# Kernel optimization log

Measured on AMD Instinct MI355X. Metric: run time of the kernel, lower is better.

## Reference

```python
import jax, jax.numpy as jnp
import numpy as np

B, S, H, L, NH, V = 8, 512, 768, 12, 12, 21128
DH = H // NH
FF = 4 * H
PAD_ID, SEP_ID = 0, 102
EPS = 1e-12


def _ln(x, g, b):
    mu = jnp.mean(x, axis=-1, keepdims=True)
    var = jnp.mean(jnp.square(x - mu), axis=-1, keepdims=True)
    return (x - mu) * jax.lax.rsqrt(var + EPS) * g + b


def setup_inputs() -> dict:
    key = jax.random.key(0)
    ks = jax.random.split(key, 24)
    # token ids with a per-sample [SEP] boundary and trailing padding
    ids = jax.random.randint(ks[0], (B, S), 1, V)
    qpos = jax.random.randint(ks[1], (B,), 16, 64)
    seqlen = jax.random.randint(ks[2], (B,), 384, S + 1)
    pos = jnp.arange(S)
    ids = jnp.where(pos[None, :] == qpos[:, None], SEP_ID, ids)
    ids = jnp.where(pos[None, :] < seqlen[:, None], ids, PAD_ID)

    w = lambda k, shape: (jax.random.normal(k, shape, dtype=jnp.float32) * 0.02)
    return {
        "input_ids": ids,
        "word_emb": w(ks[3], (V, H)),
        "pos_emb": w(ks[4], (S, H)),
        "type_emb": w(ks[5], (2, H)),
        "emb_ln_g": jnp.ones((H,), jnp.float32),
        "emb_ln_b": jnp.zeros((H,), jnp.float32),
        "attn_w": w(ks[6], (L, 4, H, H)),     # q,k,v,o projections
        "attn_b": w(ks[7], (L, 4, H)),
        "ln1_g": jnp.ones((L, H), jnp.float32),
        "ln1_b": jnp.zeros((L, H), jnp.float32),
        "ffn_w1": w(ks[8], (L, H, FF)),
        "ffn_b1": w(ks[9], (L, FF)),
        "ffn_w2": w(ks[10], (L, FF, H)),
        "ffn_b2": w(ks[11], (L, H)),
        "ln2_g": jnp.ones((L, H), jnp.float32),
        "ln2_b": jnp.zeros((L, H), jnp.float32),
        "cls_w": w(ks[12], (H, V)),
        "cls_b": jnp.zeros((V,), jnp.float32),
    }


def _qa_causal_bias(input_ids):
    # Faithful to make_qa_causal_mask: pad mask * (bidirectional over question,
    # causal over answer), boundary = first [SEP] position + 1 per sample.
    pad = input_ids != PAD_ID                                  # [B,S]
    qlen = jnp.argmax(input_ids == SEP_ID, axis=1) + 1          # [B]
    i = jnp.arange(S)[:, None]
    j = jnp.arange(S)[None, :]
    in_answer = (i[None] >= qlen[:, None, None]) & (j[None] >= qlen[:, None, None])
    causal_ok = jnp.where(in_answer, j <= i, True)              # [B,S,S]
    mask = pad[:, :, None] & pad[:, None, :] & causal_ok
    return jnp.where(mask, 0.0, -1e9).astype(jnp.float32)       # additive bias


def reference(input_ids, word_emb, pos_emb, type_emb, emb_ln_g, emb_ln_b,
              attn_w, attn_b, ln1_g, ln1_b, ffn_w1, ffn_b1, ffn_w2, ffn_b2,
              ln2_g, ln2_b, cls_w, cls_b):
    bias = _qa_causal_bias(input_ids)[:, None]                  # [B,1,S,S]
    h = word_emb[input_ids] + pos_emb[None, :S] + type_emb[0]
    h = _ln(h, emb_ln_g, emb_ln_b)
    scale = 1.0 / jnp.sqrt(jnp.float32(DH))
    for l in range(L):
        wq, wk, wv, wo = attn_w[l]
        bq, bk, bv, bo = attn_b[l]
        q = (h @ wq + bq).reshape(B, S, NH, DH)
        k = (h @ wk + bk).reshape(B, S, NH, DH)
        v = (h @ wv + bv).reshape(B, S, NH, DH)
        scores = jnp.einsum('bqhd,bkhd->bhqk', q, k) * scale + bias
        probs = jax.nn.softmax(scores, axis=-1)
        ctx = jnp.einsum('bhqk,bkhd->bqhd', probs, v).reshape(B, S, H)
        h = _ln(h + ctx @ wo + bo, ln1_g[l], ln1_b[l])
        ff = jax.nn.gelu(h @ ffn_w1[l] + ffn_b1[l], approximate=False) @ ffn_w2[l] + ffn_b2[l]
        h = _ln(h + ff, ln2_g[l], ln2_b[l])
    return h @ cls_w + cls_b                                    # [B,S,V] logits
```

## Files before the change

kernel.cpp:

```cpp
#include <hip/hip_runtime.h>
#include <hip/hip_bf16.h>
#include <stdint.h>

#define BB   8
#define SS   512
#define HH   768
#define LL   12
#define NHH  12
#define DHH  64
#define FFF  3072
#define VV   21128
#define PAD_ID 0
#define SEP_ID 102
#define BS   (BB*SS)
#define BSH  ((size_t)BS*HH)
#define BSFF ((size_t)BS*FFF)
#define QKVN (3*HH)

using bf16 = __hip_bfloat16;
typedef __attribute__((ext_vector_type(8))) short short8;
typedef __attribute__((ext_vector_type(4))) short short4v;
typedef __attribute__((ext_vector_type(4))) float f32x4;

__device__ __forceinline__ f32x4 Z4() { f32x4 z = {0.f, 0.f, 0.f, 0.f}; return z; }

__device__ __forceinline__ void gload16(void* lds, const void* g) {
    __builtin_amdgcn_global_load_lds(
        (const __attribute__((address_space(1))) uint32_t*)g,
        (__attribute__((address_space(3))) uint32_t*)(uint32_t)(uintptr_t)lds,
        16, 0, 0);
}

template <int N>
__device__ __forceinline__ void waitvm() {
    if constexpr (N == 0) asm volatile("s_waitcnt vmcnt(0)" ::: "memory");
    else if constexpr (N == 2) asm volatile("s_waitcnt vmcnt(2)" ::: "memory");
    else if constexpr (N == 3) asm volatile("s_waitcnt vmcnt(3)" ::: "memory");
    else if constexpr (N == 4) asm volatile("s_waitcnt vmcnt(4)" ::: "memory");
    else if constexpr (N == 6) asm volatile("s_waitcnt vmcnt(6)" ::: "memory");
    else asm volatile("s_waitcnt vmcnt(8)" ::: "memory");
    __builtin_amdgcn_sched_barrier(0);
}

__device__ __forceinline__ void barrier_raw() {
    __builtin_amdgcn_s_barrier();
    __builtin_amdgcn_sched_barrier(0);
}

__device__ __forceinline__ void wait_vm0_lgkm0_barrier() {
    asm volatile("s_waitcnt vmcnt(0) lgkmcnt(0)" ::: "memory");
    __builtin_amdgcn_sched_barrier(0);
    __builtin_amdgcn_s_barrier();
    __builtin_amdgcn_sched_barrier(0);
}

__global__ void __launch_bounds__(256) qlen_kernel(const int* __restrict__ ids,
                                                   int* __restrict__ qlen) {
    int b = blockIdx.x, tid = threadIdx.x;
    __shared__ int red[256];
    int best = 1 << 30;
    for (int j = tid; j < SS; j += 256)
        if (ids[b * SS + j] == SEP_ID) best = min(best, j);
    red[tid] = best; __syncthreads();
    for (int off = 128; off > 0; off >>= 1) {
        if (tid < off) red[tid] = min(red[tid], red[tid + off]);
        __syncthreads();
    }
    if (tid == 0) qlen[b] = (red[0] == (1 << 30) ? 0 : red[0]) + 1;
}

__device__ __forceinline__ float block_reduce_sum(float v, float* red, int tid) {
    red[tid] = v; __syncthreads();
    for (int off = 128; off > 0; off >>= 1) {
        if (tid < off) red[tid] += red[tid + off];
        __syncthreads();
    }
    float r = red[0]; __syncthreads();
    return r;
}

__global__ void __launch_bounds__(256) embed_ln_kernel(
    const int* __restrict__ ids, const float* __restrict__ we,
    const float* __restrict__ pe, const float* __restrict__ te,
    const float* __restrict__ g, const float* __restrict__ bt,
    float* __restrict__ h, bf16* __restrict__ hb) {
    int token = blockIdx.x, tid = threadIdx.x;
    int s = token % SS;
    int id = ids[token];
    __shared__ float red[256];
    float x[3];
#pragma unroll
    for (int i = 0; i < 3; ++i) {
        int idx = tid + i * 256;
        x[i] = we[(size_t)id * HH + idx] + pe[(size_t)s * HH + idx] + te[idx];
    }
    float sum = block_reduce_sum(x[0] + x[1] + x[2], red, tid);
    float mu = sum * (1.0f / HH);
    float vs = 0.f;
#pragma unroll
    for (int i = 0; i < 3; ++i) { float d = x[i] - mu; vs += d * d; }
    vs = block_reduce_sum(vs, red, tid);
    float rstd = rsqrtf(vs * (1.0f / HH) + 1e-12f);
    size_t base = (size_t)token * HH;
#pragma unroll
    for (int i = 0; i < 3; ++i) {
        int idx = tid + i * 256;
        float v = (x[i] - mu) * rstd * g[idx] + bt[idx];
        h[base + idx] = v;
        hb[base + idx] = __float2bfloat16(v);
    }
}

__global__ void __launch_bounds__(256) add_ln_kernel(
    float* __restrict__ h, const float* __restrict__ proj,
    const float* __restrict__ proj2,
    const float* __restrict__ g, const float* __restrict__ bt,
    bf16* __restrict__ hb) {
    int token = blockIdx.x, tid = threadIdx.x;
    __shared__ float red[256];
    size_t base = (size_t)token * HH;
    float x[3];
#pragma unroll
    for (int i = 0; i < 3; ++i) {
        int idx = tid + i * 256;
        x[i] = h[base + idx] + proj[base + idx] + proj2[base + idx];
    }
    float sum = block_reduce_sum(x[0] + x[1] + x[2], red, tid);
    float mu = sum * (1.0f / HH);
    float vs = 0.f;
#pragma unroll
    for (int i = 0; i < 3; ++i) { float d = x[i] - mu; vs += d * d; }
    vs = block_reduce_sum(vs, red, tid);
    float rstd = rsqrtf(vs * (1.0f / HH) + 1e-12f);
#pragma unroll
    for (int i = 0; i < 3; ++i) {
        int idx = tid + i * 256;
        float v = (x[i] - mu) * rstd * g[idx] + bt[idx];
        h[base + idx] = v;
        hb[base + idx] = __float2bfloat16(v);
    }
}

__global__ void __launch_bounds__(256) transp_conv(
    const float* __restrict__ in, bf16* __restrict__ out,
    int K, int N, size_t inStride, size_t outStride) {
    const float* src = in + (size_t)blockIdx.z * inStride;
    bf16* dst = out + (size_t)blockIdx.z * outStride;
    __shared__ float t[64][65];
    int n0 = blockIdx.x * 64, k0 = blockIdx.y * 64;
    int tid = threadIdx.x;
    int r = tid >> 4, c4 = (tid & 15) * 4;
#pragma unroll
    for (int i = 0; i < 4; ++i) {
        int kk = k0 + r + i * 16;
        int n = n0 + c4;
        float4 v;
        if (n + 3 < N) {
            v = *(const float4*)(src + (size_t)kk * N + n);
        } else {
            v.x = (n + 0 < N) ? src[(size_t)kk * N + n + 0] : 0.f;
            v.y = (n + 1 < N) ? src[(size_t)kk * N + n + 1] : 0.f;
            v.z = (n + 2 < N) ? src[(size_t)kk * N + n + 2] : 0.f;
            v.w = (n + 3 < N) ? src[(size_t)kk * N + n + 3] : 0.f;
        }
        t[c4 + 0][r + i * 16] = v.x;
        t[c4 + 1][r + i * 16] = v.y;
        t[c4 + 2][r + i * 16] = v.z;
        t[c4 + 3][r + i * 16] = v.w;
    }
    __syncthreads();
#pragma unroll
    for (int i = 0; i < 4; ++i) {
        int nn = n0 + r + i * 16;
        if (nn < N) {
            short4v o;
            o[0] = (short)__bfloat16_as_ushort(__float2bfloat16(t[r + i * 16][c4 + 0]));
            o[1] = (short)__bfloat16_as_ushort(__float2bfloat16(t[r + i * 16][c4 + 1]));
            o[2] = (short)__bfloat16_as_ushort(__float2bfloat16(t[r + i * 16][c4 + 2]));
            o[3] = (short)__bfloat16_as_ushort(__float2bfloat16(t[r + i * 16][c4 + 3]));
            *(short4v*)(dst + (size_t)nn * K + k0 + c4) = o;
        }
    }
}

__global__ void __launch_bounds__(256) vtrans_kernel(const bf16* __restrict__ v,
                                                     bf16* __restrict__ vT,
                                                     int ldv) {
    __shared__ bf16 t[64][68];
    int s0 = blockIdx.x * 64, h = blockIdx.y, b = blockIdx.z;
    int tid = threadIdx.x;
    int r = tid >> 4, c4 = (tid & 15) * 4;
#pragma unroll
    for (int i = 0; i < 4; ++i) {
        int sr = r + i * 16;
        short4v x = *(const short4v*)(v + ((size_t)(b * SS + s0 + sr)) * ldv +
                                      h * 64 + c4);
        t[c4 + 0][sr] = __ushort_as_bfloat16((unsigned short)x[0]);
        t[c4 + 1][sr] = __ushort_as_bfloat16((unsigned short)x[1]);
        t[c4 + 2][sr] = __ushort_as_bfloat16((unsigned short)x[2]);
        t[c4 + 3][sr] = __ushort_as_bfloat16((unsigned short)x[3]);
    }
    __syncthreads();
#pragma unroll
    for (int i = 0; i < 4; ++i) {
        int dr = r + i * 16;
        short4v o;
        o[0] = (short)__bfloat16_as_ushort(t[dr][c4 + 0]);
        o[1] = (short)__bfloat16_as_ushort(t[dr][c4 + 1]);
        o[2] = (short)__bfloat16_as_ushort(t[dr][c4 + 2]);
        o[3] = (short)__bfloat16_as_ushort(t[dr][c4 + 3]);
        *(short4v*)(vT + (((size_t)(b * NHH + h)) * 64 + dr) * SS + s0 + c4) = o;
    }
}

#define GBK 32

template <int THREADS, int TBM, int TBN, int OUT_BF16, int ACT, int KK,
          int LDA, int LDB, int LDC, int NN, int NSTAGES>
__global__ void __launch_bounds__(THREADS) gemm_bf16_kernel(
    const bf16* __restrict__ A, const bf16* __restrict__ BT,
    const float* __restrict__ bias, void* __restrict__ Cout, size_t zStride) {
    constexpr int WN = (THREADS == 512) ? 4 : 2;
    constexpr int WM = 2;
    constexpr int MFRAG = TBM / WM / 16;
    constexpr int NFRAG = TBN / WN / 16;
    constexpr int ABYTES = TBM * GBK * 2;
    constexpr int BBYTES = TBN * GBK * 2;
    constexpr int A_ISS = ABYTES / (THREADS * 16);
    constexpr int B_ISS = BBYTES / (THREADS * 16);
    constexpr int LPS = A_ISS + B_ISS;
    __shared__ __align__(16) char smem[NSTAGES * (ABYTES + BBYTES)];
    char* Asm = smem;
    char* Bsm = smem + NSTAGES * ABYTES;
    int tid = threadIdx.x;
    int lane = tid & 63, wid = tid >> 6;

    int zz = blockIdx.z;
    const char* Ab = (const char*)(A + (size_t)zz * KK);
    const char* Bb = (const char*)(BT + (size_t)zz * KK);

    int gN = gridDim.x, gM = gridDim.y;
    int nwg = gN * gM;
    int bid = blockIdx.y * gN + blockIdx.x;
    int swz = ((nwg & 7) == 0) ? ((bid & 7) * (nwg >> 3) + (bid >> 3)) : bid;
    int width = 8 * gN;
    int grp = swz / width, rem = swz % width;
    int gh = min(8, gM - grp * 8);
    int by = grp * 8 + rem % gh;
    int bx = rem / gh;

    int m0 = by * TBM, n0 = bx * TBN;
    int wr = (wid / WN) * (TBM / WM);
    int wc = (wid % WN) * (TBN / WN);

    f32x4 acc[MFRAG][NFRAG];
#pragma unroll
    for (int i = 0; i < MFRAG; ++i)
#pragma unroll
        for (int j = 0; j < NFRAG; ++j) acc[i][j] = Z4();

    auto stage = [&](int k0, int sel) {
#pragma unroll
        for (int i = 0; i < A_ISS; ++i) {
            int lin = tid * 16 + i * (THREADS * 16);
            int row = lin >> 6, slot = (lin >> 4) & 3;
            gload16(Asm + sel * ABYTES + lin,
                    Ab + ((size_t)(m0 + row) * LDA + k0) * 2 +
                        ((slot ^ ((row >> 1) & 3)) << 4));
        }
#pragma unroll
        for (int i = 0; i < B_ISS; ++i) {
            int lin = tid * 16 + i * (THREADS * 16);
            int row = lin >> 6, slot = (lin >> 4) & 3;
            int nr = n0 + row;
            if constexpr (NN % TBN != 0) { if (nr >= NN) nr = NN - 1; }
            gload16(Bsm + sel * BBYTES + lin,
                    Bb + ((size_t)nr * LDB + k0) * 2 +
                        ((slot ^ ((row >> 1) & 3)) << 4));
        }
    };

    constexpr int T = KK / GBK;
#pragma unroll
    for (int s = 0; s < NSTAGES - 1; ++s) stage(s * GBK, s);
    waitvm<(NSTAGES - 2) * LPS>();
    barrier_raw();

    for (int t = 0; t < T; ++t) {
        if (t + NSTAGES - 1 < T)
            stage((t + NSTAGES - 1) * GBK, (t + NSTAGES - 1) % NSTAGES);

        const char* Ar = Asm + (t % NSTAGES) * ABYTES;
        const char* Br = Bsm + (t % NSTAGES) * BBYTES;
        short8 af[MFRAG], bfr[NFRAG];
#pragma unroll
        for (int i = 0; i < MFRAG; ++i) {
            int ar = wr + i * 16 + (lane & 15);
            int slot = (lane >> 4) ^ ((ar >> 1) & 3);
            af[i] = *(const short8*)(Ar + ar * 64 + slot * 16);
        }
#pragma unroll
        for (int j = 0; j < NFRAG; ++j) {
            int br = wc + j * 16 + (lane & 15);
            int slot = (lane >> 4) ^ ((br >> 1) & 3);
            bfr[j] = *(const short8*)(Br + br * 64 + slot * 16);
        }
#pragma unroll
        for (int i = 0; i < MFRAG; ++i)
#pragma unroll
            for (int j = 0; j < NFRAG; ++j)
                acc[i][j] = __builtin_amdgcn_mfma_f32_16x16x32_bf16(
                    af[i], bfr[j], acc[i][j], 0, 0, 0);

        if (t + 1 < T) {
            if (t + 2 < T) waitvm<LPS>();
            else           waitvm<0>();
            barrier_raw();
        }
    }

    bool nfull = (NN % TBN == 0) || (n0 + TBN <= NN);
#pragma unroll
    for (int i = 0; i < MFRAG; ++i) {
#pragma unroll
        for (int r = 0; r < 4; ++r) {
            int m = m0 + wr + i * 16 + (lane >> 4) * 4 + r;
#pragma unroll
            for (int j = 0; j < NFRAG; ++j) {
                int n = n0 + wc + j * 16 + (lane & 15);
                if (nfull || n < NN) {
                    float v = acc[i][j][r] + ((zz == 0) ? bias[n] : 0.f);
                    if (ACT) v = 0.5f * v * (1.0f + erff(v * 0.70710678118654752f));
                    if (OUT_BF16)
                        ((bf16*)Cout)[(size_t)m * LDC + n] = __float2bfloat16(v);
                    else
                        ((float*)Cout)[zz * zStride + (size_t)m * LDC + n] = v;
                }
            }
        }
    }
}

__global__ void __launch_bounds__(256) attn_mfma_kernel(
    const bf16* __restrict__ Q, const bf16* __restrict__ K,
    const bf16* __restrict__ VT, const int* __restrict__ ids,
    const int* __restrict__ qlen, bf16* __restrict__ att, int ld) {
    __shared__ __align__(16) bf16 Qs[64 * 64];
    __shared__ __align__(16) bf16 Ks[2][64 * 64];
    __shared__ __align__(16) bf16 Vs[2][64 * 64];
    __shared__ __align__(16) bf16 Ps[4 * 16 * 64];
    __shared__ float padj[2][64];

    int tid = threadIdx.x, lane = tid & 63, w = tid >> 6;
    int q0 = blockIdx.x * 64, h = blockIdx.y, b = blockIdx.z;
    int ql = qlen[b];

    const char* kbase0 = (const char*)K + ((size_t)(b * SS) * ld) * 2;
    const char* vbase0 = (const char*)VT + (((size_t)(b * NHH + h)) * 64) * SS * 2;

    auto stageKV = [&](int kv0, int sel) {
        int lin = tid * 16;
#pragma unroll
        for (int i = 0; i < 2; ++i, lin += 4096) {
            int row = lin >> 7, bir = lin & 127;
            int sbir = bir ^ ((row & 7) << 4);
            gload16((char*)Ks[sel] + lin,
                    kbase0 + (size_t)(kv0 + row) * (ld * 2) + h * 128 + sbir);
            gload16((char*)Vs[sel] + lin,
                    vbase0 + (size_t)row * (SS * 2) + (size_t)kv0 * 2 + sbir);
        }
        if (tid < 64)
            padj[sel][tid] = (ids[b * SS + kv0 + tid] != PAD_ID) ? 1.f : 0.f;
    };

    {
        const char* qbase =
            (const char*)Q + ((size_t)(b * SS + q0) * ld) * 2 + h * 128;
        int lin = tid * 16;
#pragma unroll
        for (int i = 0; i < 2; ++i, lin += 4096) {
            int row = lin >> 7, bir = lin & 127;
            int sbir = bir ^ ((row & 7) << 4);
            gload16((char*)Qs + lin, qbase + (size_t)row * (ld * 2) + sbir);
        }
    }
    stageKV(0, 0);
    int qrow_base = q0 + w * 16 + (lane >> 4) * 4;
    bool padq[4];
#pragma unroll
    for (int r = 0; r < 4; ++r)
        padq[r] = (ids[b * SS + qrow_base + r] != PAD_ID);

    wait_vm0_lgkm0_barrier();

    short8 aq[2];
#pragma unroll
    for (int ks = 0; ks < 2; ++ks) {
        int row = w * 16 + (lane & 15);
        int bir = ks * 64 + (lane >> 4) * 16;
        aq[ks] = *(const short8*)((const char*)Qs + row * 128 +
                                  (bir ^ ((row & 7) << 4)));
    }

    float m_run[4], l_run[4];
    f32x4 accO[4];
#pragma unroll
    for (int r = 0; r < 4; ++r) { m_run[r] = -1e30f; l_run[r] = 0.f; }
#pragma unroll
    for (int d = 0; d < 4; ++d) accO[d] = Z4();

    int cur = 0;
    for (int kv0 = 0; kv0 < SS; kv0 += 64) {
        if (kv0 + 64 < SS) stageKV(kv0 + 64, cur ^ 1);
        const char* kb = (const char*)Ks[cur];
        const char* vb = (const char*)Vs[cur];

        f32x4 accS[4];
        __builtin_amdgcn_s_setprio(1);
#pragma unroll
        for (int nf = 0; nf < 4; ++nf) {
            f32x4 z = Z4();
#pragma unroll
            for (int ks = 0; ks < 2; ++ks) {
                int row = nf * 16 + (lane & 15);
                int bir = ks * 64 + (lane >> 4) * 16;
                short8 bk = *(const short8*)(kb + row * 128 +
                                             (bir ^ ((row & 7) << 4)));
                z = __builtin_amdgcn_mfma_f32_16x16x32_bf16(aq[ks], bk, z, 0, 0, 0);
            }
            accS[nf] = z;
        }
        __builtin_amdgcn_s_setprio(0);

        float p[4][4];
#pragma unroll
        for (int r = 0; r < 4; ++r) {
            int qg = qrow_base + r;
            float mx = -1e30f;
#pragma unroll
            for (int nf = 0; nf < 4; ++nf) {
                int j = kv0 + nf * 16 + (lane & 15);
                bool ok = padq[r] && (padj[cur][nf * 16 + (lane & 15)] != 0.f) &&
                          ((qg < ql) || (j < ql) || (j <= qg));
                float s = accS[nf][r] * 0.125f + (ok ? 0.f : -1e9f);
                p[r][nf] = s;
                mx = fmaxf(mx, s);
            }
#pragma unroll
            for (int off = 1; off < 16; off <<= 1)
                mx = fmaxf(mx, __shfl_xor(mx, off));
            float mnew = fmaxf(m_run[r], mx);
            float fac = __expf(m_run[r] - mnew);
            m_run[r] = mnew;
            float rs = 0.f;
#pragma unroll
            for (int nf = 0; nf < 4; ++nf) {
                float e = __expf(p[r][nf] - mnew);
                p[r][nf] = e;
                rs += e;
            }
#pragma unroll
            for (int off = 1; off < 16; off <<= 1)
                rs += __shfl_xor(rs, off);
            l_run[r] = l_run[r] * fac + rs;
#pragma unroll
            for (int df = 0; df < 4; ++df) accO[df][r] *= fac;
        }

#pragma unroll
        for (int r = 0; r < 4; ++r) {
            int prow = (lane >> 4) * 4 + r;
#pragma unroll
            for (int nf = 0; nf < 4; ++nf) {
                int c = nf * 16 + (lane & 15);
                int byte = (c * 2) ^ ((prow & 7) << 4);
                *(bf16*)((char*)Ps + w * 2048 + prow * 128 + byte) =
                    __float2bfloat16(p[r][nf]);
            }
        }
        asm volatile("s_waitcnt lgkmcnt(0)" ::: "memory");
        __builtin_amdgcn_sched_barrier(0);

        __builtin_amdgcn_s_setprio(1);
#pragma unroll
        for (int ks = 0; ks < 2; ++ks) {
            int prow = lane & 15;
            int bir = ks * 64 + (lane >> 4) * 16;
            short8 ap = *(const short8*)((const char*)Ps + w * 2048 + prow * 128 +
                                         (bir ^ ((prow & 7) << 4)));
#pragma unroll
            for (int df = 0; df < 4; ++df) {
                int vrow = df * 16 + (lane & 15);
                short8 bv = *(const short8*)(vb + vrow * 128 +
                                             (bir ^ ((vrow & 7) << 4)));
                accO[df] = __builtin_amdgcn_mfma_f32_16x16x32_bf16(
                    ap, bv, accO[df], 0, 0, 0);
            }
        }
        __builtin_amdgcn_s_setprio(0);

        if (kv0 + 64 < SS) wait_vm0_lgkm0_barrier();
        cur ^= 1;
    }

#pragma unroll
    for (int r = 0; r < 4; ++r) {
        int qg = qrow_base + r;
        float inv = 1.0f / l_run[r];
#pragma unroll
        for (int df = 0; df < 4; ++df) {
            int d = df * 16 + (lane & 15);
            att[((size_t)(b * SS) + qg) * HH + h * 64 + d] =
                __float2bfloat16(accO[df][r] * inv);
        }
    }
}

extern "C" void kernel_launch(void* const* d_in, const int* in_sizes, int n_in,
                              void* d_out, int out_size, void* d_ws, size_t ws_size,
                              hipStream_t stream) {
    const int*   ids      = (const int*)d_in[0];
    const float* word_emb = (const float*)d_in[1];
    const float* pos_emb  = (const float*)d_in[2];
    const float* type_emb = (const float*)d_in[3];
    const float* emb_ln_g = (const float*)d_in[4];
    const float* emb_ln_b = (const float*)d_in[5];
    const float* attn_w   = (const float*)d_in[6];
    const float* attn_b   = (const float*)d_in[7];
    const float* ln1_g    = (const float*)d_in[8];
    const float* ln1_b    = (const float*)d_in[9];
    const float* ffn_w1   = (const float*)d_in[10];
    const float* ffn_b1   = (const float*)d_in[11];
    const float* ffn_w2   = (const float*)d_in[12];
    const float* ffn_b2   = (const float*)d_in[13];
    const float* ln2_g    = (const float*)d_in[14];
    const float* ln2_b    = (const float*)d_in[15];
    const float* cls_w    = (const float*)d_in[16];
    const float* cls_b    = (const float*)d_in[17];
    float* out = (float*)d_out;

    char* base = (char*)d_ws;
    size_t off = 0;
    auto take = [&](size_t bytes) {
        char* r = base + off;
        off += (bytes + 255) & ~(size_t)255;
        return r;
    };
    float* h    = (float*)take(BSH * 4);
    float* proj = (float*)take(2 * BSH * 4);
    bf16*  qkv  = (bf16*)take((size_t)BS * QKVN * 2);
    bf16*  vT   = (bf16*)take(BSH * 2);
    bf16*  attb = (bf16*)take(BSH * 2);
    bf16*  ffb  = (bf16*)take(BSFF * 2);
    bf16*  hb   = (bf16*)take(BSH * 2);
    int*   qlen = (int*)take(256);
    size_t commonEnd = off;

    const size_t szAttnW = (size_t)48 * HH * HH * 2;
    const size_t szW1    = (size_t)LL * HH * FFF * 2;
    const size_t szCls   = (size_t)VV * HH * 2;
    const size_t fullNeed = commonEnd + szAttnW + 2 * szW1 + szCls;
    bool fullMode = (ws_size >= fullNeed);

    bf16 *wAttnT = nullptr, *w1T = nullptr, *w2T = nullptr, *clsT = nullptr, *wrot = nullptr;
    if (fullMode) {
        wAttnT = (bf16*)take(szAttnW);
        w1T    = (bf16*)take(szW1);
        w2T    = (bf16*)take(szW1);
        clsT   = (bf16*)take(szCls);
    } else {
        wrot = (bf16*)take((size_t)HH * FFF * 2);
        clsT = (bf16*)proj;
    }

    auto convw = [&](const float* src, bf16* dst, int K, int N) {
        dim3 g((N + 63) / 64, K / 64, 1);
        transp_conv<<<g, 256, 0, stream>>>(src, dst, K, N, (size_t)0, (size_t)0);
    };

    qlen_kernel<<<BB, 256, 0, stream>>>(ids, qlen);

    if (fullMode) {
        transp_conv<<<dim3(12, 12, 48), 256, 0, stream>>>(
            attn_w, wAttnT, HH, HH, (size_t)HH * HH, (size_t)HH * HH);
        transp_conv<<<dim3(FFF / 64, HH / 64, LL), 256, 0, stream>>>(
            ffn_w1, w1T, HH, FFF, (size_t)HH * FFF, (size_t)HH * FFF);
        transp_conv<<<dim3(HH / 64, FFF / 64, LL), 256, 0, stream>>>(
            ffn_w2, w2T, FFF, HH, (size_t)HH * FFF, (size_t)HH * FFF);
        transp_conv<<<dim3((VV + 63) / 64, HH / 64, 1), 256, 0, stream>>>(
            cls_w, clsT, HH, VV, (size_t)0, (size_t)0);
    }

    embed_ln_kernel<<<BS, 256, 0, stream>>>(ids, word_emb, pos_emb, type_emb,
                                            emb_ln_g, emb_ln_b, h, hb);

    dim3 gQKV(QKVN / 128, BS / 128, 1);
    dim3 gWo(HH / 64, BS / 128, 2);
    dim3 gFF1(FFF / 128, BS / 128, 1);
    dim3 gFF2(HH / 64, BS / 128, 2);
    dim3 gCls((VV + 127) / 128, BS / 128, 1);
    dim3 gAttn(SS / 64, NHH, BB);
    dim3 gVT(SS / 64, NHH, BB);

    for (int l = 0; l < LL; ++l) {
        const float* wq32 = attn_w + (size_t)l * 4 * HH * HH;
        const float* wo32 = wq32 + (size_t)3 * HH * HH;
        const float* bqkv = attn_b + (size_t)l * 4 * HH;
        const float* bo   = bqkv + 3 * HH;

        bf16 *wqkvT, *woT, *w1Tl, *w2Tl;
        if (fullMode) {
            wqkvT = wAttnT + (size_t)(l * 4) * HH * HH;
            woT   = wAttnT + (size_t)(l * 4 + 3) * HH * HH;
            w1Tl  = w1T + (size_t)l * HH * FFF;
            w2Tl  = w2T + (size_t)l * HH * FFF;
        } else {
            wqkvT = woT = w1Tl = w2Tl = wrot;
        }

        if (!fullMode) {
            convw(wq32, wrot, HH, HH);
            convw(wq32 + (size_t)HH * HH, wrot + (size_t)HH * HH, HH, HH);
            convw(wq32 + (size_t)2 * HH * HH, wrot + (size_t)2 * HH * HH, HH, HH);
        }
        gemm_bf16_kernel<512, 128, 128, 1, 0, HH, HH, HH, QKVN, QKVN, 3>
            <<<gQKV, 512, 0, stream>>>(hb, wqkvT, bqkv, qkv, 0);

        vtrans_kernel<<<gVT, 256, 0, stream>>>(qkv + 2 * HH, vT, QKVN);
        attn_mfma_kernel<<<gAttn, 256, 0, stream>>>(
            qkv, qkv + HH, vT, ids, qlen, attb, QKVN);

        if (!fullMode) convw(wo32, wrot, HH, HH);
        gemm_bf16_kernel<256, 128, 64, 0, 0, HH / 2, HH, HH, HH, HH, 3>
            <<<gWo, 256, 0, stream>>>(attb, woT, bo, proj, BSH);
        add_ln_kernel<<<BS, 256, 0, stream>>>(h, proj, proj + BSH,
                                              ln1_g + (size_t)l * HH,
                                              ln1_b + (size_t)l * HH, hb);

        if (!fullMode) convw(ffn_w1 + (size_t)l * HH * FFF, wrot, HH, FFF);
        gemm_bf16_kernel<512, 128, 128, 1, 1, HH, HH, HH, FFF, FFF, 3>
            <<<gFF1, 512, 0, stream>>>(hb, w1Tl, ffn_b1 + (size_t)l * FFF, ffb, 0);
        if (!fullMode) convw(ffn_w2 + (size_t)l * HH * FFF, wrot, FFF, HH);
        gemm_bf16_kernel<256, 128, 64, 0, 0, FFF / 2, FFF, FFF, HH, HH, 3>
            <<<gFF2, 256, 0, stream>>>(ffb, w2Tl, ffn_b2 + (size_t)l * HH, proj,
                                       BSH);
        add_ln_kernel<<<BS, 256, 0, stream>>>(h, proj, proj + BSH,
                                              ln2_g + (size_t)l * HH,
                                              ln2_b + (size_t)l * HH, hb);
    }

    if (!fullMode) convw(cls_w, clsT, HH, VV);
    gemm_bf16_kernel<512, 128, 128, 0, 0, HH, HH, HH, VV, VV, 3>
        <<<gCls, 512, 0, stream>>>(hb, clsT, cls_b, out, 0);
}
```

Before: 2.638 ms.

## Add 256x256-tile bf16 GEMM kernel for QKV, FFN1 and classifier projections

Introduces a new GEMM kernel with 256x256 output tiles, BK=64, double-buffered XOR-swizzled LDS, grouped block swizzling for L2 locality, and staged loads interleaved with MFMA phases. It replaces the 128x128 kernel for the QKV, FFN1 and classifier GEMMs to raise arithmetic intensity and cut global/LDS traffic per FLOP. The trade-offs are 128KB of LDS per block and large accumulator register use, fewer blocks for the smaller GEMMs (QKV yields only 144 blocks), and some wasted tile work on the ragged vocab edge.

```diff
diff --git a/kernel.cpp b/kernel.cpp
--- a/kernel.cpp
+++ b/kernel.cpp
@@ -211,6 +211,129 @@
         o[3] = (short)__bfloat16_as_ushort(t[dr][c4 + 3]);
         *(short4v*)(vT + (((size_t)(b * NHH + h)) * 64 + dr) * SS + s0 + c4) = o;
     }
+}
+
+template <int OUT_BF16, int ACT, int KK, int LDA, int LDB, int LDC, int NN>
+__global__ void __launch_bounds__(512, 2) gemm256_kernel(
+    const bf16* __restrict__ A, const bf16* __restrict__ BT,
+    const float* __restrict__ bias, void* __restrict__ Cout) {
+    __shared__ __align__(16) char smem[2 * 65536];
+    int tid = threadIdx.x, lane = tid & 63, wid = tid >> 6;
+    int mg = wid >> 2, ng = wid & 3;
+
+    int gN = gridDim.x, gM = gridDim.y;
+    int nwg = gN * gM;
+    int bid = blockIdx.y * gN + blockIdx.x;
+    int swz = ((nwg & 7) == 0) ? ((bid & 7) * (nwg >> 3) + (bid >> 3)) : bid;
+    int width = 8 * gN;
+    int grp = swz / width, rem = swz % width;
+    int gh = min(8, gM - grp * 8);
+    int by = grp * 8 + rem % gh;
+    int bx = rem / gh;
+    int m0 = by * 256, n0 = bx * 256;
+
+    const char* Ab = (const char*)A;
+    const char* Bb = (const char*)BT;
+
+    f32x4 acc[4][2][4];
+#pragma unroll
+    for (int p = 0; p < 4; ++p)
+#pragma unroll
+        for (int i = 0; i < 2; ++i)
+#pragma unroll
+            for (int j = 0; j < 4; ++j) acc[p][i][j] = Z4();
+
+    auto stageChunk = [&](int k0, int sel, int ch) {
+        const bool isB = (ch & 1);
+        const int hr0 = (ch >> 1) * 128;
+        char* base = smem + sel * 65536 + (isB ? 32768 : 0) + hr0 * 128;
+#pragma unroll
+        for (int i = 0; i < 2; ++i) {
+            int lin = tid * 16 + i * 8192;
+            int srow = hr0 + (lin >> 7);
+            int so = ((((lin >> 4) & 7) ^ (srow & 7)) << 4);
+            if (!isB) {
+                gload16(base + lin,
+                        Ab + ((size_t)(m0 + srow) * LDA + k0) * 2 + so);
+            } else {
+                int nr = n0 + srow;
+                if constexpr (NN % 256 != 0) { if (nr >= NN) nr = NN - 1; }
+                gload16(base + lin,
+                        Bb + ((size_t)nr * LDB + k0) * 2 + so);
+            }
+        }
+    };
+
+    auto ldfrag = [&](const char* buf, int row, int ks) -> short8 {
+        int slot = ks * 4 + (lane >> 4);
+        return *(const short8*)(buf + row * 128 + ((slot ^ (row & 7)) << 4));
+    };
+
+    constexpr int T = KK / 64;
+#pragma unroll
+    for (int ch = 0; ch < 4; ++ch) stageChunk(0, 0, ch);
+
+    for (int t = 0; t < T; ++t) {
+        const char* Abuf = smem + (t & 1) * 65536;
+        const char* Bbuf = Abuf + 32768;
+        short8 bfr[4][2];
+#pragma unroll
+        for (int p = 0; p < 4; ++p) {
+            if (p == 0) waitvm<0>();
+            barrier_raw();
+            short8 af[2][2];
+#pragma unroll
+            for (int i = 0; i < 2; ++i)
+#pragma unroll
+                for (int ks = 0; ks < 2; ++ks)
+                    af[i][ks] = ldfrag(
+                        Abuf, mg * 128 + p * 32 + i * 16 + (lane & 15), ks);
+            if (p == 0) {
+#pragma unroll
+                for (int j = 0; j < 4; ++j)
+#pragma unroll
+                    for (int ks = 0; ks < 2; ++ks)
+                        bfr[j][ks] = ldfrag(
+                            Bbuf, ng * 64 + j * 16 + (lane & 15), ks);
+            }
+            if (t + 1 < T) stageChunk((t + 1) * 64, (t + 1) & 1, p);
+            asm volatile("s_waitcnt lgkmcnt(0)" ::: "memory");
+            __builtin_amdgcn_sched_barrier(0);
+            __builtin_amdgcn_s_setprio(1);
+#pragma unroll
+            for (int ks = 0; ks < 2; ++ks)
+#pragma unroll
+                for (int i = 0; i < 2; ++i)
+#pragma unroll
+                    for (int j = 0; j < 4; ++j)
+                        acc[p][i][j] = __builtin_amdgcn_mfma_f32_16x16x32_bf16(
+                            af[i][ks], bfr[j][ks], acc[p][i][j], 0, 0, 0);
+            __builtin_amdgcn_s_setprio(0);
+        }
+    }
+
+#pragma unroll
+    for (int p = 0; p < 4; ++p)
+#pragma unroll
+        for (int i = 0; i < 2; ++i)
+#pragma unroll
+            for (int r = 0; r < 4; ++r) {
+                int m = m0 + mg * 128 + p * 32 + i * 16 + (lane >> 4) * 4 + r;
+#pragma unroll
+                for (int j = 0; j < 4; ++j) {
+                    int n = n0 + ng * 64 + j * 16 + (lane & 15);
+                    if ((NN % 256 == 0) || n < NN) {
+                        float v = acc[p][i][j][r] + bias[n];
+                        if (ACT)
+                            v = 0.5f * v * (1.0f + erff(v * 0.70710678118654752f));
+                        if (OUT_BF16)
+                            ((bf16*)Cout)[(size_t)m * LDC + n] =
+                                __float2bfloat16(v);
+                        else
+                            ((float*)Cout)[(size_t)m * LDC + n] = v;
+                    }
+                }
+            }
 }
 
 #define GBK 32
@@ -594,11 +717,11 @@
     embed_ln_kernel<<<BS, 256, 0, stream>>>(ids, word_emb, pos_emb, type_emb,
                                             emb_ln_g, emb_ln_b, h, hb);
 
-    dim3 gQKV(QKVN / 128, BS / 128, 1);
+    dim3 gQKV(QKVN / 256, BS / 256, 1);
     dim3 gWo(HH / 64, BS / 128, 2);
-    dim3 gFF1(FFF / 128, BS / 128, 1);
+    dim3 gFF1(FFF / 256, BS / 256, 1);
     dim3 gFF2(HH / 64, BS / 128, 2);
-    dim3 gCls((VV + 127) / 128, BS / 128, 1);
+    dim3 gCls((VV + 255) / 256, BS / 256, 1);
     dim3 gAttn(SS / 64, NHH, BB);
     dim3 gVT(SS / 64, NHH, BB);
 
@@ -623,8 +746,8 @@
             convw(wq32 + (size_t)HH * HH, wrot + (size_t)HH * HH, HH, HH);
             convw(wq32 + (size_t)2 * HH * HH, wrot + (size_t)2 * HH * HH, HH, HH);
         }
-        gemm_bf16_kernel<512, 128, 128, 1, 0, HH, HH, HH, QKVN, QKVN, 3>
-            <<<gQKV, 512, 0, stream>>>(hb, wqkvT, bqkv, qkv, 0);
+        gemm256_kernel<1, 0, HH, HH, HH, QKVN, QKVN>
+            <<<gQKV, 512, 0, stream>>>(hb, wqkvT, bqkv, qkv);
 
         vtrans_kernel<<<gVT, 256, 0, stream>>>(qkv + 2 * HH, vT, QKVN);
         attn_mfma_kernel<<<gAttn, 256, 0, stream>>>(
@@ -638,8 +761,8 @@
                                               ln1_b + (size_t)l * HH, hb);
 
         if (!fullMode) convw(ffn_w1 + (size_t)l * HH * FFF, wrot, HH, FFF);
-        gemm_bf16_kernel<512, 128, 128, 1, 1, HH, HH, HH, FFF, FFF, 3>
-            <<<gFF1, 512, 0, stream>>>(hb, w1Tl, ffn_b1 + (size_t)l * FFF, ffb, 0);
+        gemm256_kernel<1, 1, HH, HH, HH, FFF, FFF>
+            <<<gFF1, 512, 0, stream>>>(hb, w1Tl, ffn_b1 + (size_t)l * FFF, ffb);
         if (!fullMode) convw(ffn_w2 + (size_t)l * HH * FFF, wrot, FFF, HH);
         gemm_bf16_kernel<256, 128, 64, 0, 0, FFF / 2, FFF, FFF, HH, HH, 3>
             <<<gFF2, 256, 0, stream>>>(ffb, w2Tl, ffn_b2 + (size_t)l * HH, proj,
@@ -650,6 +773,6 @@
     }
 
     if (!fullMode) convw(cls_w, clsT, HH, VV);
-    gemm_bf16_kernel<512, 128, 128, 0, 0, HH, HH, HH, VV, VV, 3>
-        <<<gCls, 512, 0, stream>>>(hb, clsT, cls_b, out, 0);
-}
+    gemm256_kernel<0, 0, HH, HH, HH, VV, VV>
+        <<<gCls, 512, 0, stream>>>(hb, clsT, cls_b, out);
+}
```

After: 2.692 ms. +2.1%, slower.

## Add 256x256 four-stage GEMM for classifier and wave-per-token add+LayerNorm

Applied to the files above, without the earlier changes.

Adds a dedicated GEMM kernel with 256x256 output tiles, a 4-buffer cp-async style pipeline, XOR-swizzled LDS and grouped block swizzling, and uses it for the large vocabulary classifier projection. Larger tiles raise arithmetic intensity and cut redundant A/B loads for the big N=21128 output. Separately, the add+LayerNorm kernel now handles one token per wavefront with float4 loads and shuffle reductions instead of block-level shared-memory reductions. The bigger tile uses more LDS and registers, which limits occupancy to one block per CU, and the ragged N edge is handled with clamped loads and masked stores.

```diff
diff --git a/kernel.cpp b/kernel.cpp
--- a/kernel.cpp
+++ b/kernel.cpp
@@ -116,28 +116,46 @@
     const float* __restrict__ proj2,
     const float* __restrict__ g, const float* __restrict__ bt,
     bf16* __restrict__ hb) {
-    int token = blockIdx.x, tid = threadIdx.x;
-    __shared__ float red[256];
-    size_t base = (size_t)token * HH;
-    float x[3];
+    int tid = threadIdx.x, lane = tid & 63, w = tid >> 6;
+    size_t token = (size_t)blockIdx.x * 4 + w;
+    size_t base = token * HH;
+    f32x4 x[3];
+    float s = 0.f;
 #pragma unroll
     for (int i = 0; i < 3; ++i) {
-        int idx = tid + i * 256;
-        x[i] = h[base + idx] + proj[base + idx] + proj2[base + idx];
-    }
-    float sum = block_reduce_sum(x[0] + x[1] + x[2], red, tid);
-    float mu = sum * (1.0f / HH);
+        int j = (lane + i * 64) * 4;
+        f32x4 a = *(const f32x4*)(h + base + j);
+        f32x4 b = *(const f32x4*)(proj + base + j);
+        f32x4 c = *(const f32x4*)(proj2 + base + j);
+        f32x4 v = a + b + c;
+        x[i] = v;
+        s += v[0] + v[1] + v[2] + v[3];
+    }
+#pragma unroll
+    for (int off = 1; off < 64; off <<= 1) s += __shfl_xor(s, off);
+    float mu = s * (1.0f / HH);
     float vs = 0.f;
 #pragma unroll
-    for (int i = 0; i < 3; ++i) { float d = x[i] - mu; vs += d * d; }
-    vs = block_reduce_sum(vs, red, tid);
+    for (int i = 0; i < 3; ++i)
+#pragma unroll
+        for (int e = 0; e < 4; ++e) { float d = x[i][e] - mu; vs += d * d; }
+#pragma unroll
+    for (int off = 1; off < 64; off <<= 1) vs += __shfl_xor(vs, off);
     float rstd = rsqrtf(vs * (1.0f / HH) + 1e-12f);
 #pragma unroll
     for (int i = 0; i < 3; ++i) {
-        int idx = tid + i * 256;
-        float v = (x[i] - mu) * rstd * g[idx] + bt[idx];
-        h[base + idx] = v;
-        hb[base + idx] = __float2bfloat16(v);
+        int j = (lane + i * 64) * 4;
+        f32x4 gg = *(const f32x4*)(g + j);
+        f32x4 bb = *(const f32x4*)(bt + j);
+        f32x4 y;
+        short4v yb;
+#pragma unroll
+        for (int e = 0; e < 4; ++e) {
+            y[e] = (x[i][e] - mu) * rstd * gg[e] + bb[e];
+            yb[e] = (short)__bfloat16_as_ushort(__float2bfloat16(y[e]));
+        }
+        *(f32x4*)(h + base + j) = y;
+        *(short4v*)(hb + base + j) = yb;
     }
 }
 
@@ -211,6 +229,116 @@
         o[3] = (short)__bfloat16_as_ushort(t[dr][c4 + 3]);
         *(short4v*)(vT + (((size_t)(b * NHH + h)) * 64 + dr) * SS + s0 + c4) = o;
     }
+}
+
+template <int KK, int LDA, int LDB, int LDC, int NN>
+__global__ void __launch_bounds__(512, 1) gemm256k_kernel(
+    const bf16* __restrict__ A, const bf16* __restrict__ BT,
+    const float* __restrict__ bias, float* __restrict__ Cout) {
+    constexpr int ABYTES = 256 * 64;
+    constexpr int BUF = 2 * ABYTES;
+    constexpr int LPS = 4;
+    __shared__ __align__(16) char smem[4 * BUF];
+    int tid = threadIdx.x, lane = tid & 63, wid = tid >> 6;
+    int mg = wid >> 2, ng = wid & 3;
+
+    int gN = gridDim.x, gM = gridDim.y;
+    int nwg = gN * gM;
+    int bid = blockIdx.y * gN + blockIdx.x;
+    int swz = ((nwg & 7) == 0) ? ((bid & 7) * (nwg >> 3) + (bid >> 3)) : bid;
+    int width = 8 * gN;
+    int grp = swz / width, rem = swz % width;
+    int gh = min(8, gM - grp * 8);
+    int by = grp * 8 + rem % gh;
+    int bx = rem / gh;
+    int m0 = by * 256, n0 = bx * 256;
+
+    const char* Ab = (const char*)A;
+    const char* Bb = (const char*)BT;
+
+    f32x4 acc[8][4];
+#pragma unroll
+    for (int i = 0; i < 8; ++i)
+#pragma unroll
+        for (int j = 0; j < 4; ++j) acc[i][j] = Z4();
+
+    auto stage = [&](int k0, int sel) {
+#pragma unroll
+        for (int i = 0; i < 2; ++i) {
+            int lin = tid * 16 + i * 8192;
+            int row = lin >> 6, slot = (lin >> 4) & 3;
+            gload16(smem + sel * BUF + lin,
+                    Ab + ((size_t)(m0 + row) * LDA + k0) * 2 +
+                        ((slot ^ ((row >> 1) & 3)) << 4));
+        }
+#pragma unroll
+        for (int i = 0; i < 2; ++i) {
+            int lin = tid * 16 + i * 8192;
+            int row = lin >> 6, slot = (lin >> 4) & 3;
+            int nr = n0 + row;
+            if constexpr (NN % 256 != 0) { if (nr >= NN) nr = NN - 1; }
+            gload16(smem + sel * BUF + ABYTES + lin,
+                    Bb + ((size_t)nr * LDB + k0) * 2 +
+                        ((slot ^ ((row >> 1) & 3)) << 4));
+        }
+    };
+
+    constexpr int T = KK / 32;
+    stage(0, 0);
+    stage(32, 1);
+    stage(64, 2);
+    waitvm<2 * LPS>();
+    barrier_raw();
+
+    for (int t = 0; t < T; ++t) {
+        if (t + 3 < T) stage((t + 3) * 32, (t + 3) & 3);
+
+        const char* Ar = smem + (t & 3) * BUF;
+        const char* Br = Ar + ABYTES;
+        short8 af[8], bfr[4];
+#pragma unroll
+        for (int i = 0; i < 8; ++i) {
+            int ar = mg * 128 + i * 16 + (lane & 15);
+            int slot = (lane >> 4) ^ ((ar >> 1) & 3);
+            af[i] = *(const short8*)(Ar + ar * 64 + slot * 16);
+        }
+#pragma unroll
+        for (int j = 0; j < 4; ++j) {
+            int br = ng * 64 + j * 16 + (lane & 15);
+            int slot = (lane >> 4) ^ ((br >> 1) & 3);
+            bfr[j] = *(const short8*)(Br + br * 64 + slot * 16);
+        }
+        __builtin_amdgcn_s_setprio(1);
+#pragma unroll
+        for (int i = 0; i < 8; ++i)
+#pragma unroll
+            for (int j = 0; j < 4; ++j)
+                acc[i][j] = __builtin_amdgcn_mfma_f32_16x16x32_bf16(
+                    af[i], bfr[j], acc[i][j], 0, 0, 0);
+        __builtin_amdgcn_s_setprio(0);
+
+        if (t + 1 < T) {
+            if (t + 4 < T)      waitvm<2 * LPS>();
+            else if (t + 3 < T) waitvm<LPS>();
+            else                waitvm<0>();
+            barrier_raw();
+        }
+    }
+
+#pragma unroll
+    for (int i = 0; i < 8; ++i)
+#pragma unroll
+        for (int r = 0; r < 4; ++r) {
+            int m = m0 + mg * 128 + i * 16 + (lane >> 4) * 4 + r;
+#pragma unroll
+            for (int j = 0; j < 4; ++j) {
+                int n = n0 + ng * 64 + j * 16 + (lane & 15);
+                if ((NN % 256 == 0) || n < NN) {
+                    float v = acc[i][j][r] + bias[n];
+                    Cout[(size_t)m * LDC + n] = v;
+                }
+            }
+        }
 }
 
 #define GBK 32
@@ -598,9 +726,10 @@
     dim3 gWo(HH / 64, BS / 128, 2);
     dim3 gFF1(FFF / 128, BS / 128, 1);
     dim3 gFF2(HH / 64, BS / 128, 2);
-    dim3 gCls((VV + 127) / 128, BS / 128, 1);
+    dim3 gCls((VV + 255) / 256, BS / 256, 1);
     dim3 gAttn(SS / 64, NHH, BB);
     dim3 gVT(SS / 64, NHH, BB);
+    dim3 gLN(BS / 4, 1, 1);
 
     for (int l = 0; l < LL; ++l) {
         const float* wq32 = attn_w + (size_t)l * 4 * HH * HH;
@@ -633,9 +762,9 @@
         if (!fullMode) convw(wo32, wrot, HH, HH);
         gemm_bf16_kernel<256, 128, 64, 0, 0, HH / 2, HH, HH, HH, HH, 3>
             <<<gWo, 256, 0, stream>>>(attb, woT, bo, proj, BSH);
-        add_ln_kernel<<<BS, 256, 0, stream>>>(h, proj, proj + BSH,
-                                              ln1_g + (size_t)l * HH,
-                                              ln1_b + (size_t)l * HH, hb);
+        add_ln_kernel<<<gLN, 256, 0, stream>>>(h, proj, proj + BSH,
+                                               ln1_g + (size_t)l * HH,
+                                               ln1_b + (size_t)l * HH, hb);
 
         if (!fullMode) convw(ffn_w1 + (size_t)l * HH * FFF, wrot, HH, FFF);
         gemm_bf16_kernel<512, 128, 128, 1, 1, HH, HH, HH, FFF, FFF, 3>
@@ -644,12 +773,12 @@
         gemm_bf16_kernel<256, 128, 64, 0, 0, FFF / 2, FFF, FFF, HH, HH, 3>
             <<<gFF2, 256, 0, stream>>>(ffb, w2Tl, ffn_b2 + (size_t)l * HH, proj,
                                        BSH);
-        add_ln_kernel<<<BS, 256, 0, stream>>>(h, proj, proj + BSH,
-                                              ln2_g + (size_t)l * HH,
-                                              ln2_b + (size_t)l * HH, hb);
+        add_ln_kernel<<<gLN, 256, 0, stream>>>(h, proj, proj + BSH,
+                                               ln2_g + (size_t)l * HH,
+                                               ln2_b + (size_t)l * HH, hb);
     }
 
     if (!fullMode) convw(cls_w, clsT, HH, VV);
-    gemm_bf16_kernel<512, 128, 128, 0, 0, HH, HH, HH, VV, VV, 3>
-        <<<gCls, 512, 0, stream>>>(hb, clsT, cls_b, out, 0);
-}
+    gemm256k_kernel<HH, HH, HH, VV, VV>
+        <<<gCls, 512, 0, stream>>>(hb, clsT, cls_b, out);
+}
```

Result: no change. 2.599 ms (-1.5%).
